# Kernel tuning notes

Measured on AMD Instinct MI355X. Metric: run time of the kernel, lower is better.

The kernel has to match this reference:

```python
import jax, jax.numpy as jnp
import numpy as np

BLANK = 0
NEG = -1e30  # effective -inf that avoids nan from inf - inf


def setup_inputs() -> dict:
    key = jax.random.key(0)
    k1, k2, k3, k4 = jax.random.split(key, 4)
    B, T, U, V = 8, 256, 64, 1024
    logits = jax.random.normal(k1, (B, T, U + 1, V), dtype=jnp.float32)
    targets = jax.random.randint(k2, (B, U), 1, V)          # labels (avoid blank)
    input_lengths = jax.random.randint(k3, (B,), T // 2, T + 1)
    target_lengths = jax.random.randint(k4, (B,), U // 2, U + 1)
    return {
        "logits": logits,
        "targets": targets,
        "input_lengths": input_lengths,
        "target_lengths": target_lengths,
    }


def _rnnt_loss(logits, targets, input_lengths, target_lengths):
    # logits: (B, T, U+1, V). Standard RNN-T forward (alpha) recursion:
    #   alpha[t, u] = logaddexp(alpha[t-1, u] + blank[t-1, u],
    #                           alpha[t, u-1] + y[t, u-1])
    # loss_b = -(alpha[T_b-1, U_b] + blank[T_b-1, U_b])
    B, T, U1, V = logits.shape
    U = U1 - 1
    lp = jax.nn.log_softmax(logits, axis=-1)
    blank_lp = lp[..., BLANK]                                   # (B, T, U+1)
    # emission log-prob of target label at each (t, u), u in [0, U)
    y = jnp.take_along_axis(lp[:, :, :U, :], targets[:, None, :, None], axis=-1)[..., 0]
    u_em = jnp.arange(U)
    y = jnp.where(u_em[None, None, :] < target_lengths[:, None, None], y, NEG)
    # exclusive cumsum along u: c[b, t, u] = sum_{k<u} y[b, t, k]   (B, T, U+1)
    c = jnp.concatenate([jnp.zeros((B, T, 1), lp.dtype), jnp.cumsum(y, axis=-1)], axis=-1)
    valid_u = jnp.arange(U1)[None, :] <= target_lengths[:, None]  # (B, U+1)
    # t = 0 row: alpha[0, u] = sum_{k<u} y[0, k]
    alpha0 = jnp.where(valid_u, c[:, 0, :], NEG)
    # Within a time step, alpha[t, u] = c[u] + logcumsumexp_u(a[u'] - c[u'])
    # where a[u'] = alpha[t-1, u'] + blank[t-1, u'] -> parallel over u.
    blank_seq = jnp.moveaxis(blank_lp[:, :-1, :], 1, 0)          # (T-1, B, U+1)
    c_seq = jnp.moveaxis(c[:, 1:, :], 1, 0)                      # (T-1, B, U+1)

    def step(alpha, xs):
        b_prev, c_t = xs
        a = alpha + b_prev
        z = jax.lax.associative_scan(jnp.logaddexp, a - c_t, axis=1)
        alpha_new = jnp.where(valid_u, c_t + z, NEG)
        return alpha_new, alpha_new

    _, alphas = jax.lax.scan(step, alpha0, (blank_seq, c_seq))
    all_alpha = jnp.concatenate([alpha0[None], alphas], axis=0)  # (T, B, U+1)
    bidx = jnp.arange(B)
    a_fin = all_alpha[input_lengths - 1, bidx, target_lengths]
    b_fin = blank_lp[bidx, input_lengths - 1, target_lengths]
    ll = a_fin + b_fin
    return jnp.mean(-ll)  # reduction='mean' over batch (torchaudio semantics)


def reference(logits, targets, input_lengths, target_lengths):
    return _rnnt_loss(logits, targets, input_lengths, target_lengths)
```

## Files before the change

kernel.cpp:

```cpp
#include <hip/hip_runtime.h>
#include <math.h>

#define NEG -1e30f
#define LOG2E 1.4426950408889634f
#define LN2 0.6931471805599453f

typedef long long ll;

__device__ __forceinline__ float shup1(float x, float lane0val) {
    return __int_as_float(__builtin_amdgcn_update_dpp(
        __float_as_int(lane0val), __float_as_int(x), 0x138, 0xF, 0xF, false));
}

__device__ __forceinline__ float lae2(float x, float y) {
    float m = fmaxf(x, y);
    float dm = fminf(x, y) - m;
    return m + __builtin_amdgcn_logf(1.f + __builtin_amdgcn_exp2f(dm));
}

__global__ __launch_bounds__(256) void lse_kernel(
    const float* __restrict__ logits,
    const int* __restrict__ targets,
    float* __restrict__ blank_d,
    float* __restrict__ y_d,
    int B, int T, int U, int V) {
    const int wave = threadIdx.x >> 6;
    const int lane = threadIdx.x & 63;
    const ll nrows = (ll)B * T * (U + 1);
    const ll gwave = (ll)blockIdx.x * 4 + wave;
    const ll nwaves = (ll)gridDim.x * 4;
    const int U1 = U + 1;
    const int D = T + U;

    for (ll row = gwave; row < nrows; row += nwaves) {
        const float* base = logits + row * (ll)V;
        float4 d4[4];
#pragma unroll
        for (int c = 0; c < 4; ++c)
            d4[c] = reinterpret_cast<const float4*>(base)[c * 64 + lane];
        float s = 0.f;
#pragma unroll
        for (int c = 0; c < 4; ++c) {
            s += __builtin_amdgcn_exp2f(d4[c].x * LOG2E) +
                 __builtin_amdgcn_exp2f(d4[c].y * LOG2E) +
                 __builtin_amdgcn_exp2f(d4[c].z * LOG2E) +
                 __builtin_amdgcn_exp2f(d4[c].w * LOG2E);
        }
#pragma unroll
        for (int off = 32; off; off >>= 1) s += __shfl_xor(s, off, 64);

        if (lane == 0) {
            const float l2s = __builtin_amdgcn_logf(s);
            const int u = (int)(row % U1);
            const ll bt = row / U1;
            const int b = (int)(bt / T);
            const int t = (int)(bt % T);
            blank_d[((ll)b * D + (t + u)) * U1 + u] = d4[0].x * LOG2E - l2s;
            if (u < U) {
                const int tgt = targets[b * U + u];
                y_d[((ll)b * D + (t + u)) * U + u] = base[tgt] * LOG2E - l2s;
            }
        }
    }
}

__global__ __launch_bounds__(64) void alpha_diag_kernel(
    const float* __restrict__ blank_d,
    const float* __restrict__ y_d,
    const int* __restrict__ in_len,
    const int* __restrict__ tgt_len,
    float* __restrict__ out,
    int B, int T, int U) {
    const int b = blockIdx.x;
    const int lane = threadIdx.x & 63;
    const int D = T + U;
    const int P1 = U + 1;
    const int Dm1 = D - 1;

    const int Tb = in_len[b];
    const int L = tgt_len[b];
    const float* bd = blank_d + (ll)b * D * P1;
    const float* yd = y_d + (ll)b * D * U;
    const int dstar = Tb - 1 + L;

    float val = NEG;
    float v0 = 0.f;
    const bool yok = (lane < L);

    const int R = 16;
    float bv[R], yv[R], b0[R];
#pragma unroll
    for (int s = 0; s < R; ++s) {
        int r = s; if (r > Dm1) r = Dm1;
        bv[s] = bd[r * P1 + lane + 1];
        yv[s] = yok ? yd[r * U + lane] : NEG;
        b0[s] = bd[r * P1];
    }

    int d = 1;
    for (; d + R - 1 <= dstar; d += R) {
#pragma unroll
        for (int s = 0; s < R; ++s) {
            const float pv = val;
            const float ps = shup1(pv, v0);
            val = lae2(pv + bv[s], ps + yv[s]);
            v0 += b0[s];
            int r = d + s + R - 1;
            if (r > Dm1) r = Dm1;
            bv[s] = bd[r * P1 + lane + 1];
            yv[s] = yok ? yd[r * U + lane] : NEG;
            b0[s] = bd[r * P1];
        }
    }
#pragma unroll
    for (int s = 0; s < R; ++s) {
        if (d + s <= dstar) {
            const float pv = val;
            const float ps = shup1(pv, v0);
            val = lae2(pv + bv[s], ps + yv[s]);
            v0 += b0[s];
        }
    }

    const float aL = __shfl(val, L - 1, 64);
    const float bfin = bd[(ll)dstar * P1 + L];
    if (lane == 0)
        atomicAdd(out, -LN2 * (aL + bfin) / (float)B);
}

extern "C" void kernel_launch(void* const* d_in, const int* in_sizes, int n_in,
                              void* d_out, int out_size, void* d_ws, size_t ws_size,
                              hipStream_t stream) {
    const float* logits  = (const float*)d_in[0];
    const int* targets   = (const int*)d_in[1];
    const int* in_len    = (const int*)d_in[2];
    const int* tgt_len   = (const int*)d_in[3];

    const int B = in_sizes[2];
    const int U = in_sizes[1] / B;
    const int V = 1024;
    const int T = (int)((ll)in_sizes[0] / ((ll)B * (U + 1) * V));
    const int D = T + U;

    float* blank_d = (float*)d_ws;
    float* y_d = blank_d + (ll)B * D * (U + 1);

    hipMemsetAsync(d_out, 0, sizeof(float), stream);
    hipLaunchKernelGGL(lse_kernel, dim3(2048), dim3(256), 0, stream,
                       logits, targets, blank_d, y_d, B, T, U, V);
    hipLaunchKernelGGL(alpha_diag_kernel, dim3(B), dim3(64), 0, stream,
                       blank_d, y_d, in_len, tgt_len, (float*)d_out, B, T, U);
}
```

Measured before the change: 126.5 us.

## Use one row per wave, nontemporal loads, in-register target gather, drop memset

The LSE kernel launches one wave per row instead of a grid-stride loop, loads logits with nontemporal hints, and takes the target logit from registers with a shuffle instead of a second global load. The final loss reduction replaces the memset plus atomicAdd with per-batch partials and a last-block-done counter, which removes the separate memset launch. In exchange the grid gets much larger, and correctness now depends on the counter reset in the first kernel being ordered before the second kernel runs.

Result: faster. 104.7 us, median of 2 (-17.2%).

```diff
diff --git a/kernel.cpp b/kernel.cpp
--- a/kernel.cpp
+++ b/kernel.cpp
@@ -6,6 +6,7 @@
 #define LN2 0.6931471805599453f
 
 typedef long long ll;
+typedef float f32x4 __attribute__((ext_vector_type(4)));
 
 __device__ __forceinline__ float shup1(float x, float lane0val) {
     return __int_as_float(__builtin_amdgcn_update_dpp(
@@ -18,49 +19,66 @@
     return m + __builtin_amdgcn_logf(1.f + __builtin_amdgcn_exp2f(dm));
 }
 
+__device__ __forceinline__ void st_coh(float* p, float v) {
+    __hip_atomic_store(p, v, __ATOMIC_RELAXED, __HIP_MEMORY_SCOPE_AGENT);
+}
+__device__ __forceinline__ float ld_coh(const float* p) {
+    return __hip_atomic_load(p, __ATOMIC_RELAXED, __HIP_MEMORY_SCOPE_AGENT);
+}
+
 __global__ __launch_bounds__(256) void lse_kernel(
     const float* __restrict__ logits,
     const int* __restrict__ targets,
     float* __restrict__ blank_d,
     float* __restrict__ y_d,
+    int* __restrict__ counter,
     int B, int T, int U, int V) {
+    if (blockIdx.x == 0 && threadIdx.x == 0) *counter = 0;
     const int wave = threadIdx.x >> 6;
     const int lane = threadIdx.x & 63;
+    const ll row = (ll)blockIdx.x * 4 + wave;
     const ll nrows = (ll)B * T * (U + 1);
-    const ll gwave = (ll)blockIdx.x * 4 + wave;
-    const ll nwaves = (ll)gridDim.x * 4;
+    if (row >= nrows) return;
+    const float* base = logits + row * (ll)V;
+
+    f32x4 d4[4];
+#pragma unroll
+    for (int c = 0; c < 4; ++c)
+        d4[c] = __builtin_nontemporal_load(
+            reinterpret_cast<const f32x4*>(base) + c * 64 + lane);
+    float s = 0.f;
+#pragma unroll
+    for (int c = 0; c < 4; ++c) {
+        s += __builtin_amdgcn_exp2f(d4[c].x * LOG2E) +
+             __builtin_amdgcn_exp2f(d4[c].y * LOG2E) +
+             __builtin_amdgcn_exp2f(d4[c].z * LOG2E) +
+             __builtin_amdgcn_exp2f(d4[c].w * LOG2E);
+    }
+#pragma unroll
+    for (int off = 32; off; off >>= 1) s += __shfl_xor(s, off, 64);
+
     const int U1 = U + 1;
     const int D = T + U;
+    const int u = (int)(row % U1);
+    const ll bt = row / U1;
+    const int b = (int)(bt / T);
+    const int t = (int)(bt % T);
 
-    for (ll row = gwave; row < nrows; row += nwaves) {
-        const float* base = logits + row * (ll)V;
-        float4 d4[4];
-#pragma unroll
-        for (int c = 0; c < 4; ++c)
-            d4[c] = reinterpret_cast<const float4*>(base)[c * 64 + lane];
-        float s = 0.f;
-#pragma unroll
-        for (int c = 0; c < 4; ++c) {
-            s += __builtin_amdgcn_exp2f(d4[c].x * LOG2E) +
-                 __builtin_amdgcn_exp2f(d4[c].y * LOG2E) +
-                 __builtin_amdgcn_exp2f(d4[c].z * LOG2E) +
-                 __builtin_amdgcn_exp2f(d4[c].w * LOG2E);
-        }
-#pragma unroll
-        for (int off = 32; off; off >>= 1) s += __shfl_xor(s, off, 64);
+    float ytgt = 0.f;
+    if (u < U) {
+        const int tgt = targets[b * U + u];
+        const int q = tgt >> 2;
+        const int c = q >> 6, sl = q & 63, j = tgt & 3;
+        f32x4 f = (c == 0) ? d4[0] : (c == 1) ? d4[1] : (c == 2) ? d4[2] : d4[3];
+        float v = (j == 0) ? f.x : (j == 1) ? f.y : (j == 2) ? f.z : f.w;
+        ytgt = __shfl(v, sl, 64);
+    }
 
-        if (lane == 0) {
-            const float l2s = __builtin_amdgcn_logf(s);
-            const int u = (int)(row % U1);
-            const ll bt = row / U1;
-            const int b = (int)(bt / T);
-            const int t = (int)(bt % T);
-            blank_d[((ll)b * D + (t + u)) * U1 + u] = d4[0].x * LOG2E - l2s;
-            if (u < U) {
-                const int tgt = targets[b * U + u];
-                y_d[((ll)b * D + (t + u)) * U + u] = base[tgt] * LOG2E - l2s;
-            }
-        }
+    if (lane == 0) {
+        const float l2s = __builtin_amdgcn_logf(s);
+        blank_d[((ll)b * D + (t + u)) * U1 + u] = d4[0].x * LOG2E - l2s;
+        if (u < U)
+            y_d[((ll)b * D + (t + u)) * U + u] = ytgt * LOG2E - l2s;
     }
 }
 
@@ -69,6 +87,8 @@
     const float* __restrict__ y_d,
     const int* __restrict__ in_len,
     const int* __restrict__ tgt_len,
+    float* __restrict__ partials,
+    int* __restrict__ counter,
     float* __restrict__ out,
     int B, int T, int U) {
     const int b = blockIdx.x;
@@ -124,8 +144,17 @@
 
     const float aL = __shfl(val, L - 1, 64);
     const float bfin = bd[(ll)dstar * P1 + L];
-    if (lane == 0)
-        atomicAdd(out, -LN2 * (aL + bfin) / (float)B);
+    if (lane == 0) {
+        st_coh(&partials[b], aL + bfin);
+        asm volatile("s_waitcnt vmcnt(0)" ::: "memory");
+        const int old = __hip_atomic_fetch_add(counter, 1, __ATOMIC_RELAXED,
+                                               __HIP_MEMORY_SCOPE_AGENT);
+        if (old == B - 1) {
+            float ssum = 0.f;
+            for (int w = 0; w < B; ++w) ssum += ld_coh(&partials[w]);
+            out[0] = -LN2 * ssum / (float)B;
+        }
+    }
 }
 
 extern "C" void kernel_launch(void* const* d_in, const int* in_sizes, int n_in,
@@ -142,12 +171,17 @@
     const int T = (int)((ll)in_sizes[0] / ((ll)B * (U + 1) * V));
     const int D = T + U;
 
-    float* blank_d = (float*)d_ws;
+    float* partials = (float*)d_ws;
+    int* counter = (int*)(partials + 64);
+    float* blank_d = (float*)(counter + 16);
     float* y_d = blank_d + (ll)B * D * (U + 1);
 
-    hipMemsetAsync(d_out, 0, sizeof(float), stream);
-    hipLaunchKernelGGL(lse_kernel, dim3(2048), dim3(256), 0, stream,
-                       logits, targets, blank_d, y_d, B, T, U, V);
+    const ll rows = (ll)B * T * (U + 1);
+    const int blocks = (int)((rows + 3) / 4);
+
+    hipLaunchKernelGGL(lse_kernel, dim3(blocks), dim3(256), 0, stream,
+                       logits, targets, blank_d, y_d, counter, B, T, U, V);
     hipLaunchKernelGGL(alpha_diag_kernel, dim3(B), dim3(64), 0, stream,
-                       blank_d, y_d, in_len, tgt_len, (float*)d_out, B, T, U);
+                       blank_d, y_d, in_len, tgt_len, partials, counter,
+                       (float*)d_out, B, T, U);
 }
```
